# Optimization experiments

Measured on AMD Instinct MI355X. Metric: run time of the kernel, lower is better.

Reference implementation:

```python
import jax, jax.numpy as jnp
import numpy as np

N_E = 16384
SPLIT = (512, 512)
BETA = 0.25
K = 10
B = 4096


def _l2n(x):
    # F.normalize(p=2, dim=-1)
    return x * jax.lax.rsqrt(jnp.sum(x * x, axis=-1, keepdims=True) + 1e-12)


def _dist(x, y):
    return (jnp.sum(x * x, axis=1, keepdims=True)
            + jnp.sum(y * y, axis=1)
            - 2.0 * jnp.einsum('bd,nd->bn', x, y))


def _usage(idx):
    counts = jnp.zeros((N_E,), jnp.float32).at[idx.reshape(-1)].add(1.0)
    return jnp.sum(counts > 0).astype(jnp.float32) / N_E


def _soft_topk(d, emb):
    # smallest-K distances -> softmax(-values) weighted codebook mix
    neg_vals, idx = jax.lax.top_k(-d, K)            # [B, K]
    w = jax.nn.softmax(neg_vals, axis=1)            # softmax(-values)
    z_q = jnp.einsum('bk,bkd->bd', w, emb[idx])     # gather + weighted sum
    return z_q, idx


def _losses(z_q, z):
    vq = jnp.mean((z_q - jax.lax.stop_gradient(z)) ** 2)
    commit = BETA * jnp.mean((jax.lax.stop_gradient(z_q) - z) ** 2)
    return vq, commit


def setup_inputs() -> dict:
    key = jax.random.key(0)
    ks = jax.random.split(key, 5)
    u = 1.0 / N_E
    return {
        'z': jax.random.normal(ks[0], (B, sum(SPLIT)), jnp.float32),
        'w_text': jax.random.uniform(ks[1], (N_E, SPLIT[0]), jnp.float32, -u, u),
        'w_graph': jax.random.uniform(ks[2], (N_E, SPLIT[1]), jnp.float32, -u, u),
        'w_shared_text': jax.random.uniform(ks[3], (N_E, SPLIT[0]), jnp.float32, -u, u),
        'w_shared_graph': jax.random.uniform(ks[4], (N_E, SPLIT[1]), jnp.float32, -u, u),
    }


def reference(z, w_text, w_graph, w_shared_text, w_shared_graph):
    z_text, z_graph = jnp.split(z, [SPLIT[0]], axis=-1)

    # ---- shared codebook (joint text+graph distance) ----
    zt_n, zg_n = _l2n(z_text), _l2n(z_graph)
    wst_n, wsg_n = _l2n(w_shared_text), _l2n(w_shared_graph)
    d_shared = _dist(zt_n, wst_n) + 1.0 * _dist(zg_n, wsg_n)
    shared_emb = jnp.concatenate([wst_n, wsg_n], axis=-1)
    zq_s, idx_s = _soft_topk(d_shared, shared_emb)
    vq_s, com_s = _losses(zq_s, z)
    zq_s = z + jax.lax.stop_gradient(zq_s - z)      # straight-through
    usage_s = _usage(idx_s)

    # ---- text-specific codebook ----
    wt_n = _l2n(w_text)
    d_t = _dist(zt_n, wt_n)
    zq_t, idx_t = _soft_topk(d_t, wt_n)
    vq_t, com_t = _losses(zq_t, z_text)
    zq_t = z_text + jax.lax.stop_gradient(zq_t - z_text)
    usage_t = _usage(idx_t)

    # ---- graph-specific codebook ----
    wg_n = _l2n(w_graph)
    d_g = _dist(zg_n, wg_n)
    zq_g, idx_g = _soft_topk(d_g, wg_n)
    vq_g, com_g = _losses(zq_g, z_graph)
    zq_g = z_graph + jax.lax.stop_gradient(zq_g - z_graph)
    usage_g = _usage(idx_g)

    shared_text_emb, shared_graph_emb = jnp.split(zq_s, [SPLIT[0]], axis=-1)
    return (zq_s, shared_text_emb, shared_graph_emb, zq_t, zq_g,
            vq_s, com_s, vq_t, com_t, vq_g, com_g,
            usage_s, usage_t, usage_g)
```

## Files before the change

### kernel.cpp

```cpp
#include <hip/hip_runtime.h>
#include <stdint.h>

#define NE      16384
#define BATCH   4096
#define DFULL   1024
#define DHALF   512
#define TOPK    10
#define NCHUNK  16
#define CHUNK   1024
#define CPC     40
#define NCAND   (NCHUNK * CPC)
#define MRES    24
#define BETA_C  0.25f
#define CD1     ((size_t)BATCH * NCAND)

#define O1 ((size_t)BATCH * DFULL)
#define O2 (O1 + (size_t)BATCH * DHALF)
#define O3 (O2 + (size_t)BATCH * DHALF)
#define O4 (O3 + (size_t)BATCH * DHALF)
#define O5 (O4 + (size_t)BATCH * DHALF)

typedef __bf16 bf16x8 __attribute__((ext_vector_type(8)));
typedef float  f32x4  __attribute__((ext_vector_type(4)));

__device__ inline uint16_t f2bf(float f) {
    unsigned u = __float_as_uint(f);
    unsigned r = (u + 0x7FFFu + ((u >> 16) & 1u)) >> 16;
    return (uint16_t)r;
}
__device__ inline float bf2f(uint16_t u) {
    return __uint_as_float(((unsigned)u) << 16);
}
__device__ inline float dot8bf(uint4 e, const float* zp) {
    float s;
    s  = __uint_as_float(e.x << 16)          * zp[0];
    s += __uint_as_float(e.x & 0xFFFF0000u)  * zp[1];
    s += __uint_as_float(e.y << 16)          * zp[2];
    s += __uint_as_float(e.y & 0xFFFF0000u)  * zp[3];
    s += __uint_as_float(e.z << 16)          * zp[4];
    s += __uint_as_float(e.z & 0xFFFF0000u)  * zp[5];
    s += __uint_as_float(e.w << 16)          * zp[6];
    s += __uint_as_float(e.w & 0xFFFF0000u)  * zp[7];
    return s;
}

__global__ __launch_bounds__(256) void k_norm_z(const float* __restrict__ z,
                                                uint16_t* __restrict__ zn,
                                                float* __restrict__ rnzt,
                                                float* __restrict__ rnzg) {
    int b = blockIdx.x, t = threadIdx.x;
    const float4* zp = (const float4*)(z + (size_t)b * DFULL);
    float4 v = zp[t];
    float ss = v.x*v.x + v.y*v.y + v.z*v.z + v.w*v.w;
    #pragma unroll
    for (int off = 32; off; off >>= 1) ss += __shfl_xor(ss, off);
    __shared__ float red[4];
    if ((t & 63) == 0) red[t >> 6] = ss;
    __syncthreads();
    float tot = (t < 128) ? (red[0] + red[1]) : (red[2] + red[3]);
    float rn = rsqrtf(tot + 1e-12f);
    if (t == 0)   rnzt[b] = rn;
    if (t == 128) rnzg[b] = rn;
    uint16_t* o = zn + (size_t)b * DFULL + t * 4;
    o[0] = f2bf(v.x * rn); o[1] = f2bf(v.y * rn);
    o[2] = f2bf(v.z * rn); o[3] = f2bf(v.w * rn);
}

__global__ __launch_bounds__(128) void k_norm_cb_all(
    const float* __restrict__ w_st, const float* __restrict__ w_sg,
    const float* __restrict__ w_t,  const float* __restrict__ w_g,
    uint16_t* __restrict__ wsh, uint16_t* __restrict__ wt, uint16_t* __restrict__ wg,
    float* __restrict__ rns ) {
    int r = blockIdx.x, t = threadIdx.x, y = blockIdx.y;
    const float* w; uint16_t* dst; int dstld; float* rn_;
    if (y == 0)      { w = w_st; dst = wsh;       dstld = DFULL; rn_ = rns; }
    else if (y == 1) { w = w_sg; dst = wsh + 512; dstld = DFULL; rn_ = rns + NE; }
    else if (y == 2) { w = w_t;  dst = wt;        dstld = DHALF; rn_ = rns + 2 * NE; }
    else             { w = w_g;  dst = wg;        dstld = DHALF; rn_ = rns + 3 * NE; }
    const float4* wp = (const float4*)(w + (size_t)r * DHALF);
    float4 v = wp[t];
    float ss = v.x*v.x + v.y*v.y + v.z*v.z + v.w*v.w;
    #pragma unroll
    for (int off = 32; off; off >>= 1) ss += __shfl_xor(ss, off);
    __shared__ float red[2];
    if ((t & 63) == 0) red[t >> 6] = ss;
    __syncthreads();
    float rn = rsqrtf(red[0] + red[1] + 1e-12f);
    if (t == 0) rn_[r] = rn;
    uint16_t* o = dst + (size_t)r * dstld + t * 4;
    o[0] = f2bf(v.x * rn); o[1] = f2bf(v.y * rn);
    o[2] = f2bf(v.z * rn); o[3] = f2bf(v.w * rn);
}

__global__ __launch_bounds__(256, 3) void k_gemm_topk(
    const uint16_t* __restrict__ Zn,
    const uint16_t* __restrict__ wshn, const uint16_t* __restrict__ wtn,
    const uint16_t* __restrict__ wgn,
    unsigned* __restrict__ cand)
{
    __shared__ uint16_t Wsm[2][128 * 64];
    __shared__ uint16_t Zsm[2][64 * 64];

    const int tid  = threadIdx.x;
    const int lane = tid & 63;
    const int wv   = tid >> 6;
    const int wr   = wv >> 1;
    const int wc   = wv & 1;
    const int q    = lane >> 4;
    const int c    = lane & 15;
    const int rowbase  = blockIdx.y * 64;
    const int entchunk = blockIdx.x * CHUNK;
    const int gz = blockIdx.z;

    const uint16_t* Wn; int ldw, KT, zoff; unsigned* cdst;
    if (gz == 0)      { Wn = wshn; ldw = DFULL; KT = 16; zoff = 0;   cdst = cand; }
    else if (gz == 1) { Wn = wtn;  ldw = DHALF; KT = 8;  zoff = 0;   cdst = cand + CD1; }
    else              { Wn = wgn;  ldw = DHALF; KT = 8;  zoff = 512; cdst = cand + 2 * CD1; }
    const int ldz = DFULL;

    int so0, so1, so2, so3, so4, so5;
    int lo0, lo1, lo2, lo3, lo4, lo5;
    {
        int o, row, kb;
        o = (0 * 4 + wv) * 1024 + lane * 16; row = o >> 7; kb = (o & 127) ^ ((row & 7) << 4);
        so0 = row * (ldw * 2) + kb; lo0 = o;
        o = (1 * 4 + wv) * 1024 + lane * 16; row = o >> 7; kb = (o & 127) ^ ((row & 7) << 4);
        so1 = row * (ldw * 2) + kb; lo1 = o;
        o = (2 * 4 + wv) * 1024 + lane * 16; row = o >> 7; kb = (o & 127) ^ ((row & 7) << 4);
        so2 = row * (ldw * 2) + kb; lo2 = o;
        o = (3 * 4 + wv) * 1024 + lane * 16; row = o >> 7; kb = (o & 127) ^ ((row & 7) << 4);
        so3 = row * (ldw * 2) + kb; lo3 = o;
        o = (0 * 4 + wv) * 1024 + lane * 16; row = o >> 7; kb = (o & 127) ^ ((row & 7) << 4);
        so4 = row * (ldz * 2) + kb; lo4 = o;
        o = (1 * 4 + wv) * 1024 + lane * 16; row = o >> 7; kb = (o & 127) ^ ((row & 7) << 4);
        so5 = row * (ldz * 2) + kb; lo5 = o;
    }

    const char* Wbase = (const char*)Wn;
    const char* Zbase = (const char*)(Zn + zoff);

    unsigned La0 = 0, La1 = 0, La2 = 0, La3 = 0, La4 = 0;
    unsigned Lb0 = 0, Lb1 = 0, Lb2 = 0, Lb3 = 0, Lb4 = 0;

    uint4 sw0, sw1, sw2, sw3, sz0, sz1;

#define LOADG(cb2, kt2) {                                                           \
        const char* Wg = Wbase + ((size_t)(entchunk + (cb2) * 128) * ldw + (kt2) * 64) * 2; \
        const char* Zg = Zbase + ((size_t)rowbase * ldz + (kt2) * 64) * 2;          \
        sw0 = *(const uint4*)(Wg + so0);                                            \
        sw1 = *(const uint4*)(Wg + so1);                                            \
        sw2 = *(const uint4*)(Wg + so2);                                            \
        sw3 = *(const uint4*)(Wg + so3);                                            \
        sz0 = *(const uint4*)(Zg + so4);                                            \
        sz1 = *(const uint4*)(Zg + so5);                                            \
    }
#define WRITES(bufi) {                                                              \
        char* Wd = (char*)&Wsm[bufi][0];                                            \
        char* Zd = (char*)&Zsm[bufi][0];                                            \
        *(uint4*)(Wd + lo0) = sw0;                                                  \
        *(uint4*)(Wd + lo1) = sw1;                                                  \
        *(uint4*)(Wd + lo2) = sw2;                                                  \
        *(uint4*)(Wd + lo3) = sw3;                                                  \
        *(uint4*)(Zd + lo4) = sz0;                                                  \
        *(uint4*)(Zd + lo5) = sz1;                                                  \
    }

    LOADG(0, 0);
    WRITES(0);
    __syncthreads();
    int cur = 0;

    for (int cb = 0; cb < 8; ++cb) {
        f32x4 acc[4][2];
        #pragma unroll
        for (int m = 0; m < 4; ++m)
            #pragma unroll
            for (int n = 0; n < 2; ++n)
                acc[m][n] = (f32x4){0.f, 0.f, 0.f, 0.f};

        for (int kt = 0; kt < KT; ++kt) {
            int last = (kt + 1 == KT);
            int ncb = last ? cb + 1 : cb;
            int nkt = last ? 0 : kt + 1;
            int havenext = (ncb < 8);
            if (havenext) LOADG(ncb, nkt);

            const char* Wb = (const char*)&Wsm[cur][0];
            const char* Zb = (const char*)&Zsm[cur][0];
            #pragma unroll
            for (int ks = 0; ks < 2; ++ks) {
                int kb = ks * 64 + q * 16;
                bf16x8 b[2];
                #pragma unroll
                for (int n = 0; n < 2; ++n) {
                    int rb = wc * 32 + n * 16 + c;
                    b[n] = *(const bf16x8*)(Zb + rb * 128 + (kb ^ ((rb & 7) << 4)));
                }
                #pragma unroll
                for (int m = 0; m < 4; ++m) {
                    int ra = wr * 64 + m * 16 + c;
                    bf16x8 a = *(const bf16x8*)(Wb + ra * 128 + (kb ^ ((ra & 7) << 4)));
                    #pragma unroll
                    for (int n = 0; n < 2; ++n)
                        acc[m][n] = __builtin_amdgcn_mfma_f32_16x16x32_bf16(
                                        a, b[n], acc[m][n], 0, 0, 0);
                }
            }

            if (havenext) WRITES(cur ^ 1);
            __syncthreads();
            cur ^= 1;
        }

        const int entbase = entchunk + cb * 128 + wr * 64 + q * 4;
        #pragma unroll
        for (int n = 0; n < 2; ++n) {
            #pragma unroll
            for (int m = 0; m < 4; ++m) {
                #pragma unroll
                for (int i = 0; i < 4; ++i) {
                    unsigned u  = __float_as_uint(acc[m][n][i]);
                    unsigned mg = (unsigned)((int)u >> 31);
                    unsigned h  = (u >> 16) ^ (mg | 0x8000u);
                    unsigned p  = (h << 16) | (unsigned)(entbase + m * 16 + i);
                    if (n == 0) {
                        bool g0 = p > La0, g1 = p > La1, g2 = p > La2,
                             g3 = p > La3, g4 = p > La4;
                        La4 = g4 ? (g3 ? La3 : p) : La4;
                        La3 = g3 ? (g2 ? La2 : p) : La3;
                        La2 = g2 ? (g1 ? La1 : p) : La2;
                        La1 = g1 ? (g0 ? La0 : p) : La1;
                        La0 = g0 ? p : La0;
                    } else {
                        bool g0 = p > Lb0, g1 = p > Lb1, g2 = p > Lb2,
                             g3 = p > Lb3, g4 = p > Lb4;
                        Lb4 = g4 ? (g3 ? Lb3 : p) : Lb4;
                        Lb3 = g3 ? (g2 ? Lb2 : p) : Lb3;
                        Lb2 = g2 ? (g1 ? Lb1 : p) : Lb2;
                        Lb1 = g1 ? (g0 ? Lb0 : p) : Lb1;
                        Lb0 = g0 ? p : Lb0;
                    }
                }
            }
        }
    }

    {
        int grow = rowbase + wc * 32 + 0 * 16 + c;
        unsigned* dst = cdst + ((size_t)grow * NCHUNK + blockIdx.x) * CPC + wr * 20 + q * 5;
        dst[0] = La0; dst[1] = La1; dst[2] = La2; dst[3] = La3; dst[4] = La4;
        grow = rowbase + wc * 32 + 1 * 16 + c;
        dst = cdst + ((size_t)grow * NCHUNK + blockIdx.x) * CPC + wr * 20 + q * 5;
        dst[0] = Lb0; dst[1] = Lb1; dst[2] = Lb2; dst[3] = Lb3; dst[4] = Lb4;
    }
#undef LOADG
#undef WRITES
}

__global__ __launch_bounds__(256) void k_merge_all(
    const unsigned* __restrict__ cand,
    const uint16_t* __restrict__ wshn, const uint16_t* __restrict__ wtn,
    const uint16_t* __restrict__ wgn,
    const float* __restrict__ rnzt, const float* __restrict__ rnzg,
    const float* __restrict__ z, float* __restrict__ out,
    unsigned int* __restrict__ bm, float* __restrict__ ls)
{
    const int b = blockIdx.x, g = blockIdx.y, tid = threadIdx.x;
    const int lane = tid & 63, wv = tid >> 6;

    const unsigned* cd; const uint16_t* emb;
    int zoff, ld;
    float *outm, *outs1, *outs2;
    float rz0, rz1;
    if (g == 0) {
        cd = cand;           emb = wshn; zoff = 0;   ld = DFULL;
        outm = out; outs1 = out + O1; outs2 = out + O2;
        rz0 = rnzt[b]; rz1 = rnzg[b];
    } else if (g == 1) {
        cd = cand + CD1;     emb = wtn;  zoff = 0;   ld = DHALF;
        outm = out + O3; outs1 = nullptr; outs2 = nullptr;
        rz0 = rnzt[b]; rz1 = 0.f;
    } else {
        cd = cand + 2 * CD1; emb = wgn;  zoff = 512; ld = DHALF;
        outm = out + O4; outs1 = nullptr; outs2 = nullptr;
        rz0 = rnzg[b]; rz1 = 0.f;
    }
    unsigned int* bitmap = bm + g * (NE / 32);
    float* lossacc = ls + g;

    __shared__ float zsh[DFULL];
    __shared__ unsigned scand[MRES];
    __shared__ float ssh[MRES];
    __shared__ float wts[TOPK];
    __shared__ int   ish[TOPK];
    __shared__ float serr[4];

    const float* zrow = z + (size_t)b * DFULL + zoff;
    for (int cc = tid; cc < ld / 4; cc += 256)
        ((float4*)zsh)[cc] = ((const float4*)zrow)[cc];

    if (wv == 0) {
        unsigned creg[10];
        const unsigned* cb_ = cd + (size_t)b * NCAND;
        #pragma unroll
        for (int j = 0; j < 10; ++j) creg[j] = cb_[lane + 64 * j];
        for (int k = 0; k < MRES; ++k) {
            unsigned bv = 0;
            #pragma unroll
            for (int j = 0; j < 10; ++j) bv = (creg[j] > bv) ? creg[j] : bv;
            #pragma unroll
            for (int off = 32; off; off >>= 1) {
                unsigned ov = __shfl_xor(bv, off);
                bv = (ov > bv) ? ov : bv;
            }
            #pragma unroll
            for (int j = 0; j < 10; ++j) if (creg[j] == bv) creg[j] = 0u;
            if (lane == 0) scand[k] = bv;
        }
    }
    __syncthreads();

    for (int cc = wv; cc < MRES; cc += 4) {
        int idx = scand[cc] & 0xFFFFu;
        const uint16_t* er = emb + (size_t)idx * ld;
        uint4 e0 = *(const uint4*)(er + lane * 8);
        float t = rz0 * dot8bf(e0, zsh + lane * 8);
        if (ld == DFULL) {
            uint4 e1 = *(const uint4*)(er + 512 + lane * 8);
            t += rz1 * dot8bf(e1, zsh + 512 + lane * 8);
        }
        #pragma unroll
        for (int off = 32; off; off >>= 1) t += __shfl_xor(t, off);
        if (lane == 0) ssh[cc] = t;
    }
    __syncthreads();

    if (wv == 0) {
        float val = (lane < MRES) ? ssh[lane] : -1e30f;
        float vk[TOPK]; int sk[TOPK];
        #pragma unroll
        for (int k = 0; k < TOPK; ++k) {
            float v = val; int who = lane;
            #pragma unroll
            for (int off = 32; off; off >>= 1) {
                float ov = __shfl_xor(v, off);
                int   ow = __shfl_xor(who, off);
                if (ov > v || (ov == v && ow < who)) { v = ov; who = ow; }
            }
            vk[k] = v; sk[k] = who;
            if (lane == who) val = -1e30f;
        }
        if (lane == 0) {
            float vmax = vk[0], e[TOPK], sum = 0.f;
            #pragma unroll
            for (int k = 0; k < TOPK; ++k) { e[k] = expf(2.f * (vk[k] - vmax)); sum += e[k]; }
            #pragma unroll
            for (int k = 0; k < TOPK; ++k) {
                float w = e[k] / sum;
                int idx = scand[sk[k]] & 0xFFFFu;
                ish[k] = idx;
                wts[k] = w;
                atomicOr(&bitmap[idx >> 5], 1u << (idx & 31));
            }
        }
    }
    __syncthreads();

    float wk[TOPK]; int ik[TOPK];
    #pragma unroll
    for (int k = 0; k < TOPK; ++k) { wk[k] = wts[k]; ik[k] = ish[k]; }

    float err = 0.f;
    const int ng = ld / 4;
    for (int g2 = tid; g2 < ng; g2 += 256) {
        float ax = 0.f, ay = 0.f, az = 0.f, aw = 0.f;
        #pragma unroll
        for (int k = 0; k < TOPK; ++k) {
            ushort4 e = ((const ushort4*)(emb + (size_t)ik[k] * ld))[g2];
            float wv_ = wk[k];
            ax += wv_ * bf2f(e.x); ay += wv_ * bf2f(e.y);
            az += wv_ * bf2f(e.z); aw += wv_ * bf2f(e.w);
        }
        float4 zz = ((const float4*)zsh)[g2];
        float dx = ax - zz.x, dy = ay - zz.y, dz_ = az - zz.z, dw = aw - zz.w;
        err += dx*dx + dy*dy + dz_*dz_ + dw*dw;
        float4 a4 = {ax, ay, az, aw};
        ((float4*)(outm + (size_t)b * ld))[g2] = a4;
        if (outs1) {
            if (g2 < 128) ((float4*)(outs1 + (size_t)b * DHALF))[g2] = a4;
            else          ((float4*)(outs2 + (size_t)b * DHALF))[g2 - 128] = a4;
        }
    }
    #pragma unroll
    for (int off = 32; off; off >>= 1) err += __shfl_xor(err, off);
    if (lane == 0) serr[wv] = err;
    __syncthreads();
    if (tid == 0) atomicAdd(lossacc, serr[0] + serr[1] + serr[2] + serr[3]);
}

__global__ __launch_bounds__(256) void k_scalars(const unsigned int* __restrict__ bm,
                                                 const float* __restrict__ lossacc,
                                                 float* __restrict__ out)
{
    __shared__ float red[4];
    int tid = threadIdx.x;
    float counts[3];
    for (int g = 0; g < 3; ++g) {
        unsigned c = 0;
        for (int w = tid; w < NE / 32; w += 256) c += __popc(bm[g * (NE / 32) + w]);
        float f = (float)c;
        #pragma unroll
        for (int off = 32; off; off >>= 1) f += __shfl_xor(f, off);
        if ((tid & 63) == 0) red[tid >> 6] = f;
        __syncthreads();
        counts[g] = red[0] + red[1] + red[2] + red[3];
        __syncthreads();
    }
    if (tid == 0) {
        float vq_s = lossacc[0] / (4096.f * 1024.f);
        float vq_t = lossacc[1] / (4096.f * 512.f);
        float vq_g = lossacc[2] / (4096.f * 512.f);
        out[0] = vq_s; out[1] = BETA_C * vq_s;
        out[2] = vq_t; out[3] = BETA_C * vq_t;
        out[4] = vq_g; out[5] = BETA_C * vq_g;
        out[6] = counts[0] / (float)NE;
        out[7] = counts[1] / (float)NE;
        out[8] = counts[2] / (float)NE;
    }
}

extern "C" void kernel_launch(void* const* d_in, const int* in_sizes, int n_in,
                              void* d_out, int out_size, void* d_ws, size_t ws_size,
                              hipStream_t stream) {
    const float* z    = (const float*)d_in[0];
    const float* w_t  = (const float*)d_in[1];
    const float* w_g  = (const float*)d_in[2];
    const float* w_st = (const float*)d_in[3];
    const float* w_sg = (const float*)d_in[4];
    float* out = (float*)d_out;

    uint8_t* ws = (uint8_t*)d_ws;
    const size_t OFF_ZN  = 0;
    const size_t OFF_WSH = OFF_ZN  + (size_t)BATCH * DFULL * 2;
    const size_t OFF_WT  = OFF_WSH + (size_t)NE * DFULL * 2;
    const size_t OFF_WG  = OFF_WT  + (size_t)NE * DHALF * 2;
    const size_t OFF_CD  = OFF_WG  + (size_t)NE * DHALF * 2;
    const size_t OFF_RN  = OFF_CD  + (size_t)3 * BATCH * NCAND * 4;
    const size_t OFF_RNZ = OFF_RN  + (size_t)4 * NE * 4;
    const size_t OFF_BM  = OFF_RNZ + (size_t)2 * BATCH * 4;
    const size_t OFF_LS  = OFF_BM  + (size_t)3 * (NE / 8);

    uint16_t* zn   = (uint16_t*)(ws + OFF_ZN);
    uint16_t* wsh  = (uint16_t*)(ws + OFF_WSH);
    uint16_t* wt   = (uint16_t*)(ws + OFF_WT);
    uint16_t* wg   = (uint16_t*)(ws + OFF_WG);
    unsigned* cd   = (unsigned*)(ws + OFF_CD);
    float*    rns  = (float*)(ws + OFF_RN);
    float*    rnzt = (float*)(ws + OFF_RNZ);
    float*    rnzg = rnzt + BATCH;
    unsigned* bm   = (unsigned*)(ws + OFF_BM);
    float*    ls   = (float*)(ws + OFF_LS);

    hipMemsetAsync(ws + OFF_BM, 0, 3 * (NE / 8) + 64, stream);

    k_norm_z<<<BATCH, 256, 0, stream>>>(z, zn, rnzt, rnzg);
    k_norm_cb_all<<<dim3(NE, 4), 128, 0, stream>>>(w_st, w_sg, w_t, w_g,
                                                   wsh, wt, wg, rns);

    k_gemm_topk<<<dim3(NCHUNK, BATCH / 64, 3), 256, 0, stream>>>(zn, wsh, wt, wg, cd);

    k_merge_all<<<dim3(BATCH, 3), 256, 0, stream>>>(
        cd, wsh, wt, wg, rnzt, rnzg, z, out, bm, ls);

    k_scalars<<<1, 256, 0, stream>>>(bm, ls, out + O5);
}
```

Measured before the change: 646.9 us.

## Enlarge GEMM-topk block tile to 128 rows with 512 threads

Doubles the batch-row tile of the fused distance GEMM + top-k kernel from 64 to 128 rows per block and uses 8 waves (2x4) instead of 4. Each codebook tile loaded into shared memory is now reused across twice as many z rows, which halves codebook global reads per output. Shared memory per block grows and occupancy drops. The unseen inner loop and candidate write-out must also handle the new wave layout and row range, so correctness is a risk.

```diff
diff --git a/kernel.cpp b/kernel.cpp
--- a/kernel.cpp
+++ b/kernel.cpp
@@ -92,23 +92,23 @@
     o[2] = f2bf(v.z * rn); o[3] = f2bf(v.w * rn);
 }
 
-__global__ __launch_bounds__(256, 3) void k_gemm_topk(
+__global__ __launch_bounds__(512, 4) void k_gemm_topk(
     const uint16_t* __restrict__ Zn,
     const uint16_t* __restrict__ wshn, const uint16_t* __restrict__ wtn,
     const uint16_t* __restrict__ wgn,
     unsigned* __restrict__ cand)
 {
     __shared__ uint16_t Wsm[2][128 * 64];
-    __shared__ uint16_t Zsm[2][64 * 64];
+    __shared__ uint16_t Zsm[2][128 * 64];
 
     const int tid  = threadIdx.x;
     const int lane = tid & 63;
     const int wv   = tid >> 6;
-    const int wr   = wv >> 1;
-    const int wc   = wv & 1;
+    const int wr   = wv >> 2;
+    const int wc   = wv & 3;
     const int q    = lane >> 4;
     const int c    = lane & 15;
-    const int rowbase  = blockIdx.y * 64;
+    const int rowbase  = blockIdx.y * 128;
     const int entchunk = blockIdx.x * CHUNK;
     const int gz = blockIdx.z;
 
@@ -118,22 +118,16 @@
     else              { Wn = wgn;  ldw = DHALF; KT = 8;  zoff = 512; cdst = cand + 2 * CD1; }
     const int ldz = DFULL;
 
-    int so0, so1, so2, so3, so4, so5;
-    int lo0, lo1, lo2, lo3, lo4, lo5;
+    int sw_o0, sw_o1, sz_o0, sz_o1;
+    int lw_o0, lw_o1, lz_o0, lz_o1;
     {
         int o, row, kb;
-        o = (0 * 4 + wv) * 1024 + lane * 16; row = o >> 7; kb = (o & 127) ^ ((row & 7) << 4);
-        so0 = row * (ldw * 2) + kb; lo0 = o;
-        o = (1 * 4 + wv) * 1024 + lane * 16; row = o >> 7; kb = (o & 127) ^ ((row & 7) << 4);
-        so1 = row * (ldw * 2) + kb; lo1 = o;
-        o = (2 * 4 + wv) * 1024 + lane * 16; row = o >> 7; kb = (o & 127) ^ ((row & 7) << 4);
-        so2 = row * (ldw * 2) + kb; lo2 = o;
-        o = (3 * 4 + wv) * 1024 + lane * 16; row = o >> 7; kb = (o & 127) ^ ((row & 7) << 4);
-        so3 = row * (ldw * 2) + kb; lo3 = o;
-        o = (0 * 4 + wv) * 1024 + lane * 16; row = o >> 7; kb = (o & 127) ^ ((row & 7) << 4);
-        so4 = row * (ldz * 2) + kb; lo4 = o;
-        o = (1 * 4 + wv) * 1024 + lane * 16; row = o >> 7; kb = (o & 127) ^ ((row & 7) << 4);
-        so5 = row * (ldz * 2) + kb; lo5 = o;
+        o = (0 * 8 + wv) * 1024 + lane * 16; row = o >> 7; kb = (o & 127) ^ ((row & 7) << 4);
+        sw_o0 = row * (ldw * 2) + kb; lw_o0 = o;
+        sz_o0 = row * (ldz * 2) + kb; lz_o0 = o;
+        o = (1 * 8 + wv) * 1024 + lane * 16; row = o >> 7; kb = (o & 127) ^ ((row & 7) << 4);
+        sw_o1 = row * (ldw * 2) + kb; lw_o1 = o;
+        sz_o1 = row * (ldz * 2) + kb; lz_o1 = o;
     }
 
     const char* Wbase = (const char*)Wn;
@@ -142,27 +136,23 @@
     unsigned La0 = 0, La1 = 0, La2 = 0, La3 = 0, La4 = 0;
     unsigned Lb0 = 0, Lb1 = 0, Lb2 = 0, Lb3 = 0, Lb4 = 0;
 
-    uint4 sw0, sw1, sw2, sw3, sz0, sz1;
+    uint4 sw0, sw1, sz0, sz1;
 
 #define LOADG(cb2, kt2) {                                                           \
         const char* Wg = Wbase + ((size_t)(entchunk + (cb2) * 128) * ldw + (kt2) * 64) * 2; \
         const char* Zg = Zbase + ((size_t)rowbase * ldz + (kt2) * 64) * 2;          \
-        sw0 = *(const uint4*)(Wg + so0);                                            \
-        sw1 = *(const uint4*)(Wg + so1);                                            \
-        sw2 = *(const uint4*)(Wg + so2);                                            \
-        sw3 = *(const uint4*)(Wg + so3);                                            \
-        sz0 = *(const uint4*)(Zg + so4);                                            \
-        sz1 = *(const uint4*)(Zg + so5);                                            \
+        sw0 = *(const uint4*)(Wg + sw_o0);                                          \
+        sw1 = *(const uint4*)(Wg + sw_o1);                                          \
+        sz0 = *(const uint4*)(Zg + sz_o0);                                          \
+        sz1 = *(const uint4*)(Zg + sz_o1);                                          \
     }
 #define WRITES(bufi) {                                                              \
         char* Wd = (char*)&Wsm[bufi][0];                                            \
         char* Zd = (char*)&Zsm[bufi][0];                                            \
-        *(uint4*)(Wd + lo0) = sw0;                                                  \
-        *(uint4*)(Wd + lo1) = sw1;                                                  \
-        *(uint4*)(Wd + lo2) = sw2;                                                  \
-        *(uint4*)(Wd + lo3) = sw3;                                                  \
-        *(uint4*)(Zd + lo4) = sz0;                                                  \
-        *(uint4*)(Zd + lo5) = sz1;                                                  \
+        *(uint4*)(Wd + lw_o0) = sw0;                                                \
+        *(uint4*)(Wd + lw_o1) = sw1;                                                \
+        *(uint4*)(Zd + lz_o0) = sz0;                                                \
+        *(uint4*)(Zd + lz_o1) = sz1;                                                \
     }
 
     LOADG(0, 0);
@@ -467,7 +457,7 @@
     k_norm_cb_all<<<dim3(NE, 4), 128, 0, stream>>>(w_st, w_sg, w_t, w_g,
                                                    wsh, wt, wg, rns);
 
-    k_gemm_topk<<<dim3(NCHUNK, BATCH / 64, 3), 256, 0, stream>>>(zn, wsh, wt, wg, cd);
+    k_gemm_topk<<<dim3(NCHUNK, BATCH / 128, 3), 512, 0, stream>>>(zn, wsh, wt, wg, cd);
 
     k_merge_all<<<dim3(BATCH, 3), 256, 0, stream>>>(
         cd, wsh, wt, wg, rnzt, rnzg, z, out, bm, ls);
```

After: 620.4 us (median of 2 runs). 1.04x faster.
